# Optimization experiments

Hardware: AMD Instinct MI355X
Metric: run time of the kernel (lower is better)

Reference implementation:

```python
import jax, jax.numpy as jnp
import numpy as np

D_MODEL = 1024
N_HEADS = 16
D_HEAD = D_MODEL // N_HEADS


def setup_inputs() -> dict:
    key = jax.random.key(0)
    ks = jax.random.split(key, 16)
    B, S, D = 2, 2048, D_MODEL
    s = 1.0 / np.sqrt(D)
    inp = {
        "query": jax.random.normal(ks[0], (B, S, D), jnp.float32),
        "key": jax.random.normal(ks[1], (B, S, D), jnp.float32),
        "value": jax.random.normal(ks[2], (B, S, D), jnp.float32),
        "pos_embedding": jax.random.normal(ks[3], (B, S, D), jnp.float32),
        "Wq": jax.random.normal(ks[4], (D, D), jnp.float32) * s,
        "bq": jnp.zeros((D,), jnp.float32),
        "Wk": jax.random.normal(ks[5], (D, D), jnp.float32) * s,
        "bk": jnp.zeros((D,), jnp.float32),
        "Wv": jax.random.normal(ks[6], (D, D), jnp.float32) * s,
        "bv": jnp.zeros((D,), jnp.float32),
        "Wpos": jax.random.normal(ks[7], (D, D), jnp.float32) * s,
        "u_bias": jax.random.normal(ks[8], (N_HEADS, D_HEAD), jnp.float32) * s,
        "v_bias": jax.random.normal(ks[9], (N_HEADS, D_HEAD), jnp.float32) * s,
        "Wout": jax.random.normal(ks[10], (D, D), jnp.float32) * s,
        "bout": jnp.zeros((D,), jnp.float32),
    }
    return inp


def _rel_shift(pos_score):
    # Transformer-XL relative shift: pad one zero column, reshape, drop first row.
    B, H, S1, S2 = pos_score.shape
    zeros = jnp.zeros((B, H, S1, 1), pos_score.dtype)
    padded = jnp.concatenate([zeros, pos_score], axis=-1)  # [B,H,S1,S2+1]
    padded = padded.reshape(B, H, S2 + 1, S1)
    return padded[:, :, 1:].reshape(B, H, S1, S2)


def reference(query, key, value, pos_embedding, Wq, bq, Wk, bk, Wv, bv, Wpos, u_bias, v_bias, Wout, bout):
    B, S, D = query.shape
    H, dh = N_HEADS, D_HEAD
    q = (query @ Wq + bq).reshape(B, S, H, dh)            # [B,S,H,dh]
    k = (key @ Wk + bk).reshape(B, S, H, dh)              # [B,S,H,dh]
    v = (value @ Wv + bv).reshape(B, S, H, dh)            # [B,S,H,dh]
    p = (pos_embedding @ Wpos).reshape(B, S, H, dh)       # [B,S,H,dh]

    content_score = jnp.einsum('bqhd,bkhd->bhqk', q + u_bias, k)
    pos_score = jnp.einsum('bqhd,bkhd->bhqk', q + v_bias, p)
    pos_score = _rel_shift(pos_score)

    score = (content_score + pos_score) / jnp.asarray(np.sqrt(D), score_dtype := content_score.dtype)
    attn = jax.nn.softmax(score, axis=-1)                 # [B,H,S,S]
    context = jnp.einsum('bhqk,bkhd->bqhd', attn, v).reshape(B, S, D)
    out = context @ Wout + bout
    return out, attn
```

## Files before the change

### kernel.cpp

```cpp
#include <hip/hip_runtime.h>

#define S_LEN 2048
#define DM    1024
#define NH    16
#define DH    64
#define BATCH 2
#define S2    ((size_t)S_LEN * S_LEN)
#define CTXSZ ((size_t)BATCH * S_LEN * DM)

typedef _Float16 half_t;
typedef _Float16 f16x8 __attribute__((ext_vector_type(8)));
typedef float    f32x4 __attribute__((ext_vector_type(4)));

__device__ __forceinline__ void gll16(const void* g, void* l) {
  __builtin_amdgcn_global_load_lds(
      (const __attribute__((address_space(1))) void*)g,
      (__attribute__((address_space(3))) void*)l, 16, 0, 0);
}

__device__ __forceinline__ void stage_gll(half_t* lds, const half_t* src, int stride) {
  const int t = threadIdx.x, w = t >> 6, lane = t & 63;
  const int c1 = lane & 7, r8 = lane >> 3;
#pragma unroll
  for (int it = 0; it < 4; ++it) {
    int r = w * 32 + it * 8 + r8;
    const half_t* g = src + (size_t)r * stride + ((c1 ^ r8) << 3);
    gll16(g, lds + (size_t)w * 2048 + it * 512);
  }
}

__device__ __forceinline__ void mfma_block(const half_t* At, const half_t* Bt,
                                           int w, int lane, f32x4 acc[2][8]) {
  const int grp = lane >> 4, li = lane & 15;
#pragma unroll
  for (int ks = 0; ks < 2; ++ks) {
    const int chunk = ks * 4 + grp;
    f16x8 a[2], b[8];
#pragma unroll
    for (int fr = 0; fr < 2; ++fr) {
      int r = w * 32 + fr * 16 + li;
      a[fr] = *(const f16x8*)&At[(size_t)(r * 8 + (chunk ^ (r & 7))) * 8];
    }
#pragma unroll
    for (int fc = 0; fc < 8; ++fc) {
      int r = fc * 16 + li;
      b[fc] = *(const f16x8*)&Bt[(size_t)(r * 8 + (chunk ^ (r & 7))) * 8];
    }
#pragma unroll
    for (int fr = 0; fr < 2; ++fr)
#pragma unroll
      for (int fc = 0; fc < 8; ++fc)
        acc[fr][fc] = __builtin_amdgcn_mfma_f32_16x16x32_f16(a[fr], b[fc], acc[fr][fc], 0, 0, 0);
  }
}

template<typename ST>
__device__ __forceinline__ void load8s(const ST* p, float* o) {
  if constexpr (sizeof(ST) == 2) {
    f16x8 v = *(const f16x8*)p;
#pragma unroll
    for (int e = 0; e < 8; ++e) o[e] = (float)v[e];
  } else {
    const float4* q = (const float4*)p;
    float4 a = q[0], b = q[1];
    o[0]=a.x; o[1]=a.y; o[2]=a.z; o[3]=a.w; o[4]=b.x; o[5]=b.y; o[6]=b.z; o[7]=b.w;
  }
}

struct PArgs {
  const float* asrc[4]; half_t* adst[4];
  const float* wsrc[5]; half_t* wdst[5];
};

__global__ __launch_bounds__(256) void prep(PArgs pa, half_t* zbuf) {
  __shared__ float T[64][65];
  const int bx = blockIdx.x, t = threadIdx.x;
  if (bx < 8192) {
    if (bx == 0 && t < 8) {
      float4 z = {0.f, 0.f, 0.f, 0.f};
      ((float4*)zbuf)[t] = z;
    }
    const int mat = bx >> 11, blk = bx & 2047;
    const float* s = pa.asrc[mat];
    half_t* d = pa.adst[mat];
    size_t i = ((size_t)blk * 256 + t) * 8;
    float4 v0 = *(const float4*)(s + i), v1 = *(const float4*)(s + i + 4);
    f16x8 h;
    h[0]=(half_t)v0.x; h[1]=(half_t)v0.y; h[2]=(half_t)v0.z; h[3]=(half_t)v0.w;
    h[4]=(half_t)v1.x; h[5]=(half_t)v1.y; h[6]=(half_t)v1.z; h[7]=(half_t)v1.w;
    *(f16x8*)(d + i) = h;
  } else {
    const int idx = bx - 8192;
    const int z = idx >> 8, rem = idx & 255;
    const int k0 = (rem & 15) * 64, n0 = (rem >> 4) * 64;
    const float* W = pa.wsrc[z];
    half_t* D = pa.wdst[z];
#pragma unroll
    for (int it = 0; it < 4; ++it) {
      int id2 = t + it * 256; int r = id2 >> 4, c4 = (id2 & 15) * 4;
      float4 v = *(const float4*)(W + (size_t)(k0 + r) * DM + n0 + c4);
      T[r][c4] = v.x; T[r][c4 + 1] = v.y; T[r][c4 + 2] = v.z; T[r][c4 + 3] = v.w;
    }
    __syncthreads();
#pragma unroll
    for (int it = 0; it < 2; ++it) {
      int id2 = t + it * 256; int n = id2 >> 3, kc = (id2 & 7) * 8;
      f16x8 o;
#pragma unroll
      for (int e = 0; e < 8; ++e) o[e] = (half_t)T[kc + e][n];
      *(f16x8*)&D[(size_t)(n0 + n) * DM + k0 + kc] = o;
    }
  }
}

struct GArgs {
  const half_t* A[4];  const half_t* Bt[4];
  const float* ba[4]; const float* bu[4]; const float* bv[4];
  half_t* oa[4]; half_t* ob[4]; float* of[4];
};

template<bool F32OUT>
__global__ __launch_bounds__(256) void gemm_k(GArgs g, int K) {
  __shared__ __align__(16) half_t At[128 * 64];
  __shared__ __align__(16) half_t Bt[128 * 64];
  const int z = blockIdx.z;
  const half_t* A = g.A[z];
  const half_t* B = g.Bt[z];
  const int n0 = blockIdx.x * 128, m0 = blockIdx.y * 128;
  const int t = threadIdx.x, w = t >> 6, lane = t & 63;
  const f32x4 zf = {0.f, 0.f, 0.f, 0.f};
  f32x4 acc[2][8];
#pragma unroll
  for (int i = 0; i < 2; ++i)
#pragma unroll
    for (int j = 0; j < 8; ++j) acc[i][j] = zf;

  for (int k0 = 0; k0 < K; k0 += 64) {
    stage_gll(At, A + (size_t)m0 * K + k0, K);
    stage_gll(Bt, B + (size_t)n0 * K + k0, K);
    __syncthreads();
    mfma_block(At, Bt, w, lane, acc);
    __syncthreads();
  }
  const int grp = lane >> 4, li = lane & 15;
#pragma unroll
  for (int fr = 0; fr < 2; ++fr)
#pragma unroll
    for (int fc = 0; fc < 8; ++fc)
#pragma unroll
      for (int r = 0; r < 4; ++r) {
        int row = m0 + w * 32 + fr * 16 + grp * 4 + r;
        int col = n0 + fc * 16 + li;
        float v = acc[fr][fc][r];
        if (g.ba[z]) v += g.ba[z][col];
        if constexpr (F32OUT) {
          g.of[z][(size_t)row * DM + col] = v;
        } else {
          float v1 = v + (g.bu[z] ? g.bu[z][col] : 0.f);
          g.oa[z][(size_t)row * DM + col] = (half_t)v1;
          if (g.ob[z]) g.ob[z][(size_t)row * DM + col] = (half_t)(v + g.bv[z][col]);
        }
      }
}

__global__ __launch_bounds__(256) void vtrans(const half_t* vp, half_t* vT) {
  __shared__ half_t T[64][72];
  const int s0 = blockIdx.x * 64, h = blockIdx.y, b = blockIdx.z;
  const int t = threadIdx.x;
#pragma unroll
  for (int it = 0; it < 2; ++it) {
    int idx = t + it * 256; int s = idx >> 3, c = idx & 7;
    uint4 v = *(const uint4*)(vp + ((size_t)(b * S_LEN + s0 + s)) * DM + h * DH + c * 8);
    *(uint4*)&T[s][c * 8] = v;
  }
  __syncthreads();
  half_t* dst = vT + ((size_t)(b * NH + h)) * DH * S_LEN;
#pragma unroll
  for (int it = 0; it < 2; ++it) {
    int idx = t + it * 256; int d = idx >> 3, sc = (idx & 7) * 8;
    f16x8 o;
#pragma unroll
    for (int e = 0; e < 8; ++e) o[e] = T[sc + e][d];
    *(f16x8*)&dst[(size_t)d * S_LEN + s0 + sc] = o;
  }
}

template<typename ST>
__global__ __launch_bounds__(512, 6) void score_fused(
    const half_t* __restrict__ qu_, const half_t* __restrict__ qv_,
    const half_t* __restrict__ kp_, const half_t* __restrict__ pp_,
    const half_t* __restrict__ zbuf, ST* __restrict__ sc, float* __restrict__ part)
{
  __shared__ __align__(16) half_t MsR[16896];
  __shared__ __align__(16) half_t QV[128 * 64];
  half_t* QU = MsR;
  half_t* Kt = MsR + 8192;
  half_t* Ms = MsR;

  const int bh = blockIdx.z, b = bh >> 4, h = bh & 15;
  const int kt = blockIdx.x, qt = blockIdx.y;
  const int i0 = qt * 128, k0 = kt * 128;
  const int base = 1920 + k0 - i0;
  const int t = threadIdx.x, w = t >> 6, lane = t & 63;
  const int grp = lane >> 4, li = lane & 15;

  {
    const half_t* srcA = qu_ + ((size_t)(b * S_LEN + i0)) * DM + h * DH;
    const half_t* srcB = kp_ + ((size_t)(b * S_LEN + k0)) * DM + h * DH;
    const half_t* srcQ = qv_ + ((size_t)(b * S_LEN + i0)) * DM + h * DH;
#pragma unroll
    for (int p = 0; p < 2; ++p) {
      int cidx = t + p * 512; int r = cidx >> 3, c = cidx & 7;
      size_t off = (size_t)r * DM + ((c ^ (r & 7)) << 3);
      gll16(srcA + off, QU + (size_t)cidx * 8);
      gll16(srcB + off, Kt + (size_t)cidx * 8);
      gll16(srcQ + off, QV + (size_t)cidx * 8);
    }
  }

  const int e0 = w * 16 + li, e1 = (w + 8) * 16 + li;
  const int dlt0 = (base + e0 >= S_LEN + 1) ? 1 : 0;
  const int dlt1 = (base + e1 >= S_LEN + 1) ? 1 : 0;
  f16x8 bm[2][2];
#pragma unroll
  for (int eci = 0; eci < 2; ++eci) {
    int e_row = eci ? e1 : e0;
    int jv = base + e_row; if (jv >= S_LEN + 1) jv -= (S_LEN + 1);
    const half_t* srcp = (jv == S_LEN) ? zbuf
        : pp_ + ((size_t)(b * S_LEN + jv)) * DM + h * DH;
#pragma unroll
    for (int kk = 0; kk < 2; ++kk)
      bm[kk][eci] = *(const f16x8*)(srcp + (kk * 4 + grp) * 8);
  }
  __syncthreads();

  const f32x4 zf = {0.f, 0.f, 0.f, 0.f};
  f32x4 acc_c[8];
#pragma unroll
  for (int j = 0; j < 8; ++j) acc_c[j] = zf;
#pragma unroll
  for (int kk = 0; kk < 2; ++kk) {
    const int chunk = kk * 4 + grp;
    int ra = w * 16 + li;
    f16x8 a = *(const f16x8*)&QU[(size_t)(ra * 8 + (chunk ^ (ra & 7))) * 8];
#pragma unroll
    for (int fc = 0; fc < 8; ++fc) {
      int rb = fc * 16 + li;
      f16x8 bf = *(const f16x8*)&Kt[(size_t)(rb * 8 + (chunk ^ (rb & 7))) * 8];
      acc_c[fc] = __builtin_amdgcn_mfma_f32_16x16x32_f16(a, bf, acc_c[fc], 0, 0, 0);
    }
  }
  __syncthreads();

  for (int rf = 0; rf < 8; ++rf) {
    f32x4 am[2] = {zf, zf};
#pragma unroll
    for (int kk = 0; kk < 2; ++kk) {
      int ra = rf * 16 + li;
      f16x8 a = *(const f16x8*)&QV[(size_t)(ra * 8 + ((kk * 4 + grp) ^ (ra & 7))) * 8];
      am[0] = __builtin_amdgcn_mfma_f32_16x16x32_f16(a, bm[kk][0], am[0], 0, 0, 0);
      am[1] = __builtin_amdgcn_mfma_f32_16x16x32_f16(a, bm[kk][1], am[1], 0, 0, 0);
    }
#pragma unroll
    for (int eci = 0; eci < 2; ++eci) {
      int e = eci ? e1 : e0;
      int dlt = eci ? dlt1 : dlt0;
#pragma unroll
      for (int r = 0; r < 4; ++r) {
        int rM = rf * 16 + grp * 4 + r;
        int q = rM - dlt;
        int k = e + q - 127;
        if ((unsigned)q < 128u && (unsigned)k < 128u)
          Ms[q * 132 + k] = (half_t)am[eci][r];
      }
    }
  }

  {
    f16x8 aq0, aq1;
    {
      int r128 = i0 + 128; if (r128 > S_LEN - 1) r128 = S_LEN - 1;
      const half_t* q128p = qv_ + ((size_t)(b * S_LEN + r128)) * DM + h * DH;
      aq0 = *(const f16x8*)(q128p + (0 * 4 + grp) * 8);
      aq1 = *(const f16x8*)(q128p + (1 * 4 + grp) * 8);
    }
    f32x4 am0 = zf;
    am0 = __builtin_amdgcn_mfma_f32_16x16x32_f16(aq0, bm[0][0], am0, 0, 0, 0);
    am0 = __builtin_amdgcn_mfma_f32_16x16x32_f16(aq1, bm[1][0], am0, 0, 0, 0);
    if (grp == 0 && dlt0 == 1)
      Ms[127 * 132 + e0] = (half_t)am0[0];
  }
  __syncthreads();

  ST* sb = sc + (size_t)bh * S2;
  float lsum[4] = {0.f, 0.f, 0.f, 0.f};
#pragma unroll
  for (int fc = 0; fc < 8; ++fc) {
#pragma unroll
    for (int rr = 0; rr < 4; ++rr) {
      int q = w * 16 + grp * 4 + rr;
      int k = fc * 16 + li;
      float mval = (float)Ms[q * 132 + k];
      float s = (acc_c[fc][rr] + mval) * 0.03125f;
      float ev = __expf(s);
      sb[(size_t)(i0 + q) * S_LEN + k0 + k] = (ST)ev;
      lsum[rr] += ev;
    }
  }
#pragma unroll
  for (int rr = 0; rr < 4; ++rr) {
    float v = lsum[rr];
#pragma unroll
    for (int d = 1; d < 16; d <<= 1) v += __shfl_xor(v, d);
    if (li == 0)
      part[((size_t)bh * S_LEN + i0 + w * 16 + grp * 4 + rr) * 16 + kt] = v;
  }
}

template<typename ST>
__global__ __launch_bounds__(256) void av_attn(const ST* sc, const half_t* vT, const float* part,
                                               float* attn, half_t* ctx) {
  __shared__ __align__(16) half_t Vt[2][64 * 128];
  __shared__ float Ls[128];
  const int bh = blockIdx.y, b = bh >> 4, h = bh & 15;
  const int q0 = blockIdx.x * 128;
  const int t = threadIdx.x;
  if (t < 128) {
    const float* pp = part + ((size_t)bh * S_LEN + q0 + t) * 16;
    float L = 0.f;
#pragma unroll
    for (int k = 0; k < 16; ++k) L += pp[k];
    Ls[t] = 1.f / L;
  }
  const ST* sb = sc + (size_t)bh * S2;
  float* ab = attn + (size_t)bh * S2;
  const half_t* vb = vT + (size_t)bh * (DH * S_LEN);
  const int w = t >> 6, lane = t & 63, grp = lane >> 4, li = lane & 15;
  const int c1 = lane & 15, d4 = lane >> 4;
  const f32x4 zf = {0.f, 0.f, 0.f, 0.f};
  f32x4 acc[2][4];
#pragma unroll
  for (int i = 0; i < 2; ++i)
#pragma unroll
    for (int j = 0; j < 4; ++j) acc[i][j] = zf;

#pragma unroll
  for (int it = 0; it < 4; ++it) {
    int d = w * 16 + it * 4 + d4;
    gll16(vb + (size_t)d * S_LEN + ((c1 ^ (d & 15)) << 3), Vt[0] + (size_t)w * 2048 + it * 512);
  }
  __syncthreads();
  int cur = 0;

  for (int kt = 0; kt < 16; ++kt) {
    if (kt + 1 < 16) {
#pragma unroll
      for (int it = 0; it < 4; ++it) {
        int d = w * 16 + it * 4 + d4;
        gll16(vb + (size_t)d * S_LEN + (kt + 1) * 128 + ((c1 ^ (d & 15)) << 3),
              Vt[cur ^ 1] + (size_t)w * 2048 + it * 512);
      }
    }
#pragma unroll
    for (int ks = 0; ks < 4; ++ks) {
      f16x8 pa[2];
#pragma unroll
      for (int fr = 0; fr < 2; ++fr) {
        int r128 = w * 32 + fr * 16 + li;
        int row = q0 + r128;
        int col = kt * 128 + ks * 32 + grp * 8;
        float sv[8];
        load8s(&sb[(size_t)row * S_LEN + col], sv);
        float rL = Ls[r128];
#pragma unroll
        for (int e = 0; e < 8; ++e) sv[e] *= rL;
        float4* dst = (float4*)&ab[(size_t)row * S_LEN + col];
        float4 w0 = {sv[0], sv[1], sv[2], sv[3]};
        float4 w1 = {sv[4], sv[5], sv[6], sv[7]};
        dst[0] = w0; dst[1] = w1;
        f16x8 ph;
#pragma unroll
        for (int e = 0; e < 8; ++e) ph[e] = (half_t)sv[e];
        pa[fr] = ph;
      }
      f16x8 bf[4];
#pragma unroll
      for (int fc = 0; fc < 4; ++fc) {
        int d = fc * 16 + li; int chunk = ks * 4 + grp;
        bf[fc] = *(const f16x8*)&Vt[cur][(size_t)(d * 16 + (chunk ^ (d & 15))) * 8];
      }
#pragma unroll
      for (int fr = 0; fr < 2; ++fr)
#pragma unroll
        for (int fc = 0; fc < 4; ++fc)
          acc[fr][fc] = __builtin_amdgcn_mfma_f32_16x16x32_f16(pa[fr], bf[fc], acc[fr][fc], 0, 0, 0);
    }
    __syncthreads();
    cur ^= 1;
  }
#pragma unroll
  for (int fr = 0; fr < 2; ++fr)
#pragma unroll
    for (int fc = 0; fc < 4; ++fc)
#pragma unroll
      for (int r = 0; r < 4; ++r) {
        int q = q0 + w * 32 + fr * 16 + grp * 4 + r;
        int d = fc * 16 + li;
        ctx[((size_t)(b * S_LEN + q)) * DM + h * DH + d] = (half_t)acc[fr][fc][r];
      }
}

extern "C" void kernel_launch(void* const* d_in, const int* in_sizes, int n_in,
                              void* d_out, int out_size, void* d_ws, size_t ws_size,
                              hipStream_t stream) {
  (void)in_sizes; (void)n_in; (void)out_size;

  const float* query  = (const float*)d_in[0];
  const float* key    = (const float*)d_in[1];
  const float* value  = (const float*)d_in[2];
  const float* pos    = (const float*)d_in[3];
  const float* Wq     = (const float*)d_in[4];
  const float* bq     = (const float*)d_in[5];
  const float* Wk     = (const float*)d_in[6];
  const float* bk     = (const float*)d_in[7];
  const float* Wv     = (const float*)d_in[8];
  const float* bv     = (const float*)d_in[9];
  const float* Wpos   = (const float*)d_in[10];
  const float* u_bias = (const float*)d_in[11];
  const float* v_bias = (const float*)d_in[12];
  const float* Wout   = (const float*)d_in[13];
  const float* bout   = (const float*)d_in[14];

  float* out  = (float*)d_out;
  float* attn = out + (size_t)BATCH * S_LEN * DM;

  char* ws = (char*)d_ws;
  half_t* Wt   = (half_t*)(ws);
  half_t* Af16 = (half_t*)(ws + 10485760);
  float*  part = (float*)(ws + 10485760);
  half_t* qu   = (half_t*)(ws + 44040192);
  half_t* qv   = (half_t*)(ws + 52428800);
  half_t* kp   = (half_t*)(ws + 60817408);
  half_t* pp   = (half_t*)(ws + 69206016);
  half_t* vp   = (half_t*)(ws + 77594624);
  half_t* vT   = (half_t*)(ws + 85983232);
  half_t* ctx  = (half_t*)(ws + 77594624);
  half_t* zbuf = (half_t*)(ws + 94371840);
  half_t* scH  = (half_t*)(ws + 94375936);
  const bool fast = ws_size >= (size_t)94375936 + (size_t)BATCH * NH * S2 * 2;

  dim3 blk(256);

  PArgs pa;
  pa.asrc[0] = query; pa.asrc[1] = key; pa.asrc[2] = value; pa.asrc[3] = pos;
  for (int i = 0; i < 4; ++i) pa.adst[i] = Af16 + (size_t)i * CTXSZ;
  pa.wsrc[0] = Wq; pa.wsrc[1] = Wk; pa.wsrc[2] = Wv; pa.wsrc[3] = Wpos; pa.wsrc[4] = Wout;
  for (int i = 0; i < 5; ++i) pa.wdst[i] = Wt + (size_t)i * DM * DM;
  prep<<<dim3(8192 + 1280), blk, 0, stream>>>(pa, zbuf);

  GArgs ga{};
  for (int i = 0; i < 4; ++i) {
    ga.A[i]  = Af16 + (size_t)i * CTXSZ;
    ga.Bt[i] = Wt + (size_t)i * DM * DM;
  }
  ga.ba[0] = bq; ga.ba[1] = bk; ga.ba[2] = bv; ga.ba[3] = nullptr;
  ga.bu[0] = u_bias; ga.bv[0] = v_bias;
  ga.oa[0] = qu; ga.oa[1] = kp; ga.oa[2] = vp; ga.oa[3] = pp;
  ga.ob[0] = qv;
  gemm_k<false><<<dim3(8, 32, 4), blk, 0, stream>>>(ga, DM);

  vtrans<<<dim3(32, 16, 2), blk, 0, stream>>>(vp, vT);

  dim3 g_sc(16, 16, 32);
  dim3 blk5(512);
  if (fast) {
    score_fused<half_t><<<g_sc, blk5, 0, stream>>>(qu, qv, kp, pp, zbuf, scH, part);
    av_attn<half_t><<<dim3(16, 32), blk, 0, stream>>>(scH, vT, part, attn, ctx);
  } else {
    float* scF = attn;
    score_fused<float><<<g_sc, blk5, 0, stream>>>(qu, qv, kp, pp, zbuf, scF, part);
    av_attn<float><<<dim3(16, 32), blk, 0, stream>>>(scF, vT, part, attn, ctx);
  }

  GArgs go{};
  go.A[0] = ctx; go.Bt[0] = Wt + (size_t)4 * DM * DM;
  go.ba[0] = bout; go.of[0] = out;
  gemm_k<true><<<dim3(8, 32, 1), blk, 0, stream>>>(go, DM);
}
```

Before: 511.7 us.

## Swizzle GEMM workgroups across XCDs and simplify score-kernel indexing

The GEMM kernel remaps its linear block id so that consecutive tiles sharing A rows land on the same XCD, aiming for better L2 reuse. The score kernel precomputes row bounds and linear address offsets for the relative-shift scatter into LDS, replacing per-element index arithmetic and bounds checks. The exp/store loop is reordered to go row-major with base pointers hoisted, which reduces address computation. The swizzle hardcodes an 8x32 grid shape and assumes 8 XCDs.

```diff
diff --git a/kernel.cpp b/kernel.cpp
--- a/kernel.cpp
+++ b/kernel.cpp
@@ -123,10 +123,16 @@
 __global__ __launch_bounds__(256) void gemm_k(GArgs g, int K) {
   __shared__ __align__(16) half_t At[128 * 64];
   __shared__ __align__(16) half_t Bt[128 * 64];
-  const int z = blockIdx.z;
+  const int lin = blockIdx.x + 8 * (blockIdx.y + 32 * blockIdx.z);
+  const int nwg = 8 * 32 * gridDim.z;
+  const int xcd = lin & 7, tt = lin >> 3;
+  const int grpid = xcd * (nwg >> 6) + (tt >> 3);
+  const int n0 = (tt & 7) * 128;
+  const int z = grpid >> 5;
+  const int m0 = (grpid & 31) * 128;
+
   const half_t* A = g.A[z];
   const half_t* B = g.Bt[z];
-  const int n0 = blockIdx.x * 128, m0 = blockIdx.y * 128;
   const int t = threadIdx.x, w = t >> 6, lane = t & 63;
   const f32x4 zf = {0.f, 0.f, 0.f, 0.f};
   f32x4 acc[2][8];
@@ -252,6 +258,13 @@
   }
   __syncthreads();
 
+  const int C0 = e0 - 127 - 133 * dlt0;
+  const int C1 = e1 - 127 - 133 * dlt1;
+  int lo0 = 127 + dlt0 - e0; if (lo0 < dlt0) lo0 = dlt0;
+  int hi0 = 254 + dlt0 - e0; if (hi0 > 127) hi0 = 127;
+  int lo1 = 127 + dlt1 - e1; if (lo1 < dlt1) lo1 = dlt1;
+  int hi1 = 254 + dlt1 - e1; if (hi1 > 127) hi1 = 127;
+
   for (int rf = 0; rf < 8; ++rf) {
     f32x4 am[2] = {zf, zf};
 #pragma unroll
@@ -261,17 +274,21 @@
       am[0] = __builtin_amdgcn_mfma_f32_16x16x32_f16(a, bm[kk][0], am[0], 0, 0, 0);
       am[1] = __builtin_amdgcn_mfma_f32_16x16x32_f16(a, bm[kk][1], am[1], 0, 0, 0);
     }
-#pragma unroll
-    for (int eci = 0; eci < 2; ++eci) {
-      int e = eci ? e1 : e0;
-      int dlt = eci ? dlt1 : dlt0;
+    const int rMb = rf * 16 + grp * 4;
+    {
+      int addr = rMb * 133 + C0;
 #pragma unroll
       for (int r = 0; r < 4; ++r) {
-        int rM = rf * 16 + grp * 4 + r;
-        int q = rM - dlt;
-        int k = e + q - 127;
-        if ((unsigned)q < 128u && (unsigned)k < 128u)
-          Ms[q * 132 + k] = (half_t)am[eci][r];
+        int rM = rMb + r;
+        if (rM >= lo0 && rM <= hi0) Ms[addr + 133 * r] = (half_t)am[0][r];
+      }
+    }
+    {
+      int addr = rMb * 133 + C1;
+#pragma unroll
+      for (int r = 0; r < 4; ++r) {
+        int rM = rMb + r;
+        if (rM >= lo1 && rM <= hi1) Ms[addr + 133 * r] = (half_t)am[1][r];
       }
     }
   }
@@ -293,19 +310,24 @@
   __syncthreads();
 
   ST* sb = sc + (size_t)bh * S2;
-  float lsum[4] = {0.f, 0.f, 0.f, 0.f};
-#pragma unroll
-  for (int fc = 0; fc < 8; ++fc) {
-#pragma unroll
-    for (int rr = 0; rr < 4; ++rr) {
-      int q = w * 16 + grp * 4 + rr;
-      int k = fc * 16 + li;
-      float mval = (float)Ms[q * 132 + k];
+  const int qb = w * 16 + grp * 4;
+  const half_t* MsB = Ms + qb * 132 + li;
+  ST* sbB = sb + (size_t)(i0 + qb) * S_LEN + k0 + li;
+  float lsum[4];
+#pragma unroll
+  for (int rr = 0; rr < 4; ++rr) {
+    const half_t* mrow = MsB + rr * 132;
+    ST* srow = sbB + (size_t)rr * S_LEN;
+    float acc = 0.f;
+#pragma unroll
+    for (int fc = 0; fc < 8; ++fc) {
+      float mval = (float)mrow[fc * 16];
       float s = (acc_c[fc][rr] + mval) * 0.03125f;
       float ev = __expf(s);
-      sb[(size_t)(i0 + q) * S_LEN + k0 + k] = (ST)ev;
-      lsum[rr] += ev;
-    }
+      srow[fc * 16] = (ST)ev;
+      acc += ev;
+    }
+    lsum[rr] = acc;
   }
 #pragma unroll
   for (int rr = 0; rr < 4; ++rr) {
@@ -313,7 +335,7 @@
 #pragma unroll
     for (int d = 1; d < 16; d <<= 1) v += __shfl_xor(v, d);
     if (li == 0)
-      part[((size_t)bh * S_LEN + i0 + w * 16 + grp * 4 + rr) * 16 + kt] = v;
+      part[((size_t)bh * S_LEN + i0 + qb + rr) * 16 + kt] = v;
   }
 }
 
```

New measurement: 513.9 us (median of 2 runs). No clear change (+0.4%).
